# Optimization experiments

Hardware: AMD Instinct MI355X
Metric: run time of the kernel (lower is better)

Reference implementation:

```python
import jax, jax.numpy as jnp
import numpy as np

D_MODEL = 512
H = 8
D_FF = 2048
EPS = 1e-6
NEG_INF = -1.0e9


def setup_inputs() -> dict:
    key = jax.random.key(0)
    ks = jax.random.split(key, 12)
    B, S, D, F = 8, 2048, D_MODEL, D_FF
    s = 0.02
    inp = {
        "x": jax.random.normal(ks[0], (B, S, D), jnp.float32),
        "src_mask": jnp.ones((B, 1, 1, S), jnp.int32),
        "w_q": jax.random.normal(ks[1], (D, D), jnp.float32) * s,
        "b_q": jnp.zeros((D,), jnp.float32),
        "w_k": jax.random.normal(ks[2], (D, D), jnp.float32) * s,
        "b_k": jnp.zeros((D,), jnp.float32),
        "w_v": jax.random.normal(ks[3], (D, D), jnp.float32) * s,
        "b_v": jnp.zeros((D,), jnp.float32),
        "w_o": jax.random.normal(ks[4], (D, D), jnp.float32) * s,
        "b_o": jnp.zeros((D,), jnp.float32),
        "w_1": jax.random.normal(ks[5], (F, D), jnp.float32) * s,
        "b_1": jnp.zeros((F,), jnp.float32),
        "w_2": jax.random.normal(ks[6], (D, F), jnp.float32) * s,
        "b_2": jnp.zeros((D,), jnp.float32),
    }
    return inp


def _layer_norm(x):
    # Matches torch: (x - mu) / sqrt(std**2 + eps), std is UNBIASED (ddof=1);
    # alpha/bias params exist in the module but are never applied in forward.
    mu = jnp.mean(x, axis=-1, keepdims=True)
    var = jnp.var(x, axis=-1, keepdims=True, ddof=1)
    return (x - mu) / jnp.sqrt(var + EPS)


def _mha(x, src_mask, w_q, b_q, w_k, b_k, w_v, b_v, w_o, b_o):
    B, S, D = x.shape
    d_k = D // H
    q = x @ w_q.T + b_q
    k = x @ w_k.T + b_k
    v = x @ w_v.T + b_v
    # (B, S, H, d_k) -> (B, H, S, d_k)
    q = q.reshape(B, S, H, d_k).transpose(0, 2, 1, 3)
    k = k.reshape(B, S, H, d_k).transpose(0, 2, 1, 3)
    v = v.reshape(B, S, H, d_k).transpose(0, 2, 1, 3)
    scores = jnp.einsum("bhqd,bhkd->bhqk", q, k) / jnp.sqrt(jnp.float32(d_k))
    scores = jnp.where(src_mask == 0, NEG_INF, scores)
    attn = jax.nn.softmax(scores, axis=-1)  # (B, H, S, S) materialized, as in source
    out = jnp.einsum("bhqk,bhkd->bhqd", attn, v)
    out = out.transpose(0, 2, 1, 3).reshape(B, S, D)
    return out @ w_o.T + b_o


def _ffn(x, w_1, b_1, w_2, b_2):
    return jax.nn.relu(x @ w_1.T + b_1) @ w_2.T + b_2


def reference(x, src_mask, w_q, b_q, w_k, b_k, w_v, b_v, w_o, b_o, w_1, b_1, w_2, b_2):
    # dropout prob = 0.0 -> identity (eval-equivalent)
    x1 = x + _mha(_layer_norm(x), src_mask, w_q, b_q, w_k, b_k, w_v, b_v, w_o, b_o)
    return x1 + _ffn(_layer_norm(x1), w_1, b_1, w_2, b_2)
```

## Files before the change

### kernel.cpp

```cpp
#include <hip/hip_runtime.h>
#include <hip/hip_bf16.h>

typedef unsigned short u16;
typedef __bf16 bf16x8 __attribute__((ext_vector_type(8)));
typedef __bf16 bf16x4 __attribute__((ext_vector_type(4)));
typedef unsigned short u16x8 __attribute__((ext_vector_type(8)));
typedef float f32x4 __attribute__((ext_vector_type(4)));

#define SEQ 2048
#define DMODEL 512
#define NHEAD 8
#define DFF 2048
#define NBATCH 8
#define MROWS (NBATCH * SEQ)

__device__ __forceinline__ u16 f2b(float f) {
    __hip_bfloat16 h = __float2bfloat16(f);
    u16 u;
    __builtin_memcpy(&u, &h, 2);
    return u;
}

__device__ __forceinline__ float ex2(float x) {
#if __has_builtin(__builtin_amdgcn_exp2f)
    return __builtin_amdgcn_exp2f(x);
#else
    return exp2f(x);
#endif
}

__device__ __forceinline__ void gload_lds16(const void* g, void* lds) {
    auto* gp = reinterpret_cast<const __attribute__((address_space(1))) unsigned int*>(
        reinterpret_cast<uintptr_t>(g));
    auto* lp = reinterpret_cast<__attribute__((address_space(3))) unsigned int*>(
        reinterpret_cast<uintptr_t>(lds));
    __builtin_amdgcn_global_load_lds(gp, lp, 16, 0, 0);
}

__global__ __launch_bounds__(256) void cast_weights(
    const float* __restrict__ w0, const float* __restrict__ w1,
    const float* __restrict__ w2, const float* __restrict__ w3,
    const float* __restrict__ w4, const float* __restrict__ w5,
    u16* __restrict__ d0, u16* __restrict__ d1, u16* __restrict__ d2,
    u16* __restrict__ d3, u16* __restrict__ d4, u16* __restrict__ d5) {
    int blk = blockIdx.x;
    const float* s;
    u16* d;
    int base;
    if (blk < 512) {
        int seg = blk >> 7, lb = blk & 127;
        s = seg == 0 ? w0 : seg == 1 ? w1 : seg == 2 ? w2 : w3;
        d = seg == 0 ? d0 : seg == 1 ? d1 : seg == 2 ? d2 : d3;
        base = lb * 2048;
    } else if (blk < 1024) {
        s = w4; d = d4; base = (blk - 512) * 2048;
    } else {
        s = w5; d = d5; base = (blk - 1024) * 2048;
    }
    int i = base + threadIdx.x * 8;
    float4 a = *reinterpret_cast<const float4*>(s + i);
    float4 b = *reinterpret_cast<const float4*>(s + i + 4);
    ushort4 oa, ob;
    oa.x = f2b(a.x); oa.y = f2b(a.y); oa.z = f2b(a.z); oa.w = f2b(a.w);
    ob.x = f2b(b.x); ob.y = f2b(b.y); ob.z = f2b(b.z); ob.w = f2b(b.w);
    *reinterpret_cast<ushort4*>(d + i) = oa;
    *reinterpret_cast<ushort4*>(d + i + 4) = ob;
}

__global__ __launch_bounds__(256) void ln_rows(const float* __restrict__ x,
                                               u16* __restrict__ out) {
    int row = blockIdx.x * 4 + (threadIdx.x >> 6);
    int l = threadIdx.x & 63;
    const float* xr = x + (size_t)row * DMODEL + l * 8;
    float4 a = *reinterpret_cast<const float4*>(xr);
    float4 b = *reinterpret_cast<const float4*>(xr + 4);
    float s = a.x + a.y + a.z + a.w + b.x + b.y + b.z + b.w;
    float q = a.x * a.x + a.y * a.y + a.z * a.z + a.w * a.w +
              b.x * b.x + b.y * b.y + b.z * b.z + b.w * b.w;
#pragma unroll
    for (int d = 32; d >= 1; d >>= 1) {
        s += __shfl_xor(s, d, 64);
        q += __shfl_xor(q, d, 64);
    }
    float mean = s * (1.f / 512.f);
    float var = (q - 512.f * mean * mean) * (1.f / 511.f);
    float rs = rsqrtf(var + 1e-6f);
    ushort4 o0, o1;
    o0.x = f2b((a.x - mean) * rs); o0.y = f2b((a.y - mean) * rs);
    o0.z = f2b((a.z - mean) * rs); o0.w = f2b((a.w - mean) * rs);
    o1.x = f2b((b.x - mean) * rs); o1.y = f2b((b.y - mean) * rs);
    o1.z = f2b((b.z - mean) * rs); o1.w = f2b((b.w - mean) * rs);
    u16* op = out + (size_t)row * DMODEL + l * 8;
    *reinterpret_cast<ushort4*>(op) = o0;
    *reinterpret_cast<ushort4*>(op + 4) = o1;
}

template <bool RELU, bool RESID, int OUTMODE>
__global__ __launch_bounds__(256, 2) void gemm_nt(
    const u16* __restrict__ A, const u16* __restrict__ W,
    const float* __restrict__ bias, const float* __restrict__ resid,
    void* __restrict__ Cout, int N, int K) {
    __shared__ u16 Als[128 * 64];
    __shared__ u16 Bls[128 * 64];
    const int tid = threadIdx.x;
    const int l = tid & 63, w = tid >> 6;
    const int m0 = blockIdx.y * 128;
    const int n0 = blockIdx.x * 128;
    const int wr = (w >> 1) * 64, wc = (w & 1) * 64;
    const int lhi = l >> 4, l15 = l & 15, l7 = l & 7;

    f32x4 acc[4][4] = {};

    const int srow = l >> 3;
    const int scol = ((l & 7) * 8) ^ (srow << 3);

    for (int kt = 0; kt < K; kt += 64) {
        __syncthreads();
#pragma unroll
        for (int i = 0; i < 4; ++i) {
            int cc = w * 4 + i;
            int grow = cc * 8 + srow;
            gload_lds16(&A[(size_t)(m0 + grow) * K + kt + scol], &Als[cc * 512]);
            gload_lds16(&W[(size_t)(n0 + grow) * K + kt + scol], &Bls[cc * 512]);
        }
        __syncthreads();
#pragma unroll
        for (int kk = 0; kk < 2; ++kk) {
            const int koff = (kk * 32 + lhi * 8) ^ (l7 << 3);
            bf16x8 af[4], bfr[4];
#pragma unroll
            for (int m = 0; m < 4; ++m)
                af[m] = *reinterpret_cast<const bf16x8*>(
                    &Als[(wr + m * 16 + l15) * 64 + koff]);
#pragma unroll
            for (int n = 0; n < 4; ++n)
                bfr[n] = *reinterpret_cast<const bf16x8*>(
                    &Bls[(wc + n * 16 + l15) * 64 + koff]);
#pragma unroll
            for (int m = 0; m < 4; ++m)
#pragma unroll
                for (int n = 0; n < 4; ++n)
                    acc[m][n] = __builtin_amdgcn_mfma_f32_16x16x32_bf16(
                        af[m], bfr[n], acc[m][n], 0, 0, 0);
        }
    }

    int colg[4];
    float bv[4];
#pragma unroll
    for (int cn = 0; cn < 4; ++cn) {
        colg[cn] = n0 + wc + cn * 16 + l15;
        bv[cn] = bias[colg[cn]];
    }
#pragma unroll
    for (int am = 0; am < 4; ++am) {
        int rowg = m0 + wr + am * 16 + 4 * lhi;
#pragma unroll
        for (int cn = 0; cn < 4; ++cn) {
            float v[4];
#pragma unroll
            for (int r = 0; r < 4; ++r) {
                float t = acc[am][cn][r] + bv[cn];
                if constexpr (RELU) t = fmaxf(t, 0.f);
                if constexpr (RESID)
                    t += resid[(size_t)(rowg + r) * N + colg[cn]];
                v[r] = t;
            }
            if constexpr (OUTMODE == 0) {
                u16* o = (u16*)Cout;
#pragma unroll
                for (int r = 0; r < 4; ++r)
                    o[(size_t)(rowg + r) * N + colg[cn]] = f2b(v[r]);
            } else if constexpr (OUTMODE == 1) {
                float* o = (float*)Cout;
#pragma unroll
                for (int r = 0; r < 4; ++r)
                    o[(size_t)(rowg + r) * N + colg[cn]] = v[r];
            } else {
                u16* o = (u16*)Cout;
                int bb = rowg >> 11, sloc = rowg & 2047;
                ushort4 pk;
                pk.x = f2b(v[0]); pk.y = f2b(v[1]);
                pk.z = f2b(v[2]); pk.w = f2b(v[3]);
                *reinterpret_cast<ushort4*>(
                    &o[((size_t)(bb * 512 + colg[cn])) * 2048 + sloc]) = pk;
            }
        }
    }
}

__global__ __launch_bounds__(256, 3) void attn_fwd(
    const u16* __restrict__ q, const u16* __restrict__ k,
    const u16* __restrict__ vT, const int* __restrict__ mask,
    u16* __restrict__ out) {
    __shared__ u16 Kls[2][64 * 64];
    __shared__ u16 Vls[2][64 * 64];
    const int tid = threadIdx.x;
    const int l = tid & 63, w = tid >> 6;
    const int lhi = l >> 4, l15 = l & 15;
    const int lb = (blockIdx.x & 7) * 128 + (blockIdx.x >> 3);
    const int qt = lb & 15, bh = lb >> 4;
    const int b = bh >> 3, h = bh & 7;
    const int q0 = qt * 128 + w * 32;

    const u16* Kb = k + (size_t)b * SEQ * DMODEL + h * 64;
    const u16* Vb = vT + ((size_t)b * 512 + h * 64) * SEQ;
    const int* Mb = mask + b * SEQ;

    const int srow = l >> 3;
    const int scol = ((l & 7) ^ srow) << 3;

    bf16x8 qf[2][2];
#pragma unroll
    for (int g = 0; g < 2; ++g) {
        size_t qa = ((size_t)b * SEQ + q0 + g * 16 + l15) * DMODEL + h * 64 + lhi * 8;
        qf[g][0] = *reinterpret_cast<const bf16x8*>(&q[qa]);
        qf[g][1] = *reinterpret_cast<const bf16x8*>(&q[qa + 32]);
    }

    int allone;
    {
        int acc = 1;
#pragma unroll
        for (int i = 0; i < 8; ++i) {
            int4 mm = *reinterpret_cast<const int4*>(&Mb[l * 32 + i * 4]);
            acc &= mm.x & mm.y & mm.z & mm.w;
        }
        allone = __all(acc == 1);
    }

    float mrun[2] = {-1e30f, -1e30f};
    float lrun[2] = {0.f, 0.f};
    f32x4 oacc[2][4] = {};
    const float C1 = 0.18033688f;

    auto stage = [&](int buf, int kv) {
#pragma unroll
        for (int i = 0; i < 2; ++i) {
            int cc = w * 2 + i;
            int row = cc * 8 + srow;
            gload_lds16(&Kb[(size_t)(kv + row) * DMODEL + scol], &Kls[buf][cc * 512]);
            gload_lds16(&Vb[(size_t)row * SEQ + kv + scol], &Vls[buf][cc * 512]);
        }
    };

    stage(0, 0);
    asm volatile("s_waitcnt vmcnt(0)" ::: "memory");
    __builtin_amdgcn_s_barrier();

    for (int t = 0; t < 32; ++t) {
        const int buf = t & 1;
        const int kv = t * 64;
        if (t < 31) stage(buf ^ 1, kv + 64);
        __builtin_amdgcn_sched_barrier(0);

        const int sw = (l15 & 7) << 3;

        f32x4 sc[2][4];
        __builtin_amdgcn_s_setprio(1);
#pragma unroll
        for (int ks = 0; ks < 4; ++ks) {
            int krow = ks * 16 + l15;
            bf16x8 ka0 = *reinterpret_cast<const bf16x8*>(
                &Kls[buf][krow * 64 + ((lhi * 8) ^ sw)]);
            bf16x8 ka1 = *reinterpret_cast<const bf16x8*>(
                &Kls[buf][krow * 64 + ((32 + lhi * 8) ^ sw)]);
#pragma unroll
            for (int g = 0; g < 2; ++g) {
                f32x4 z = {};
                z = __builtin_amdgcn_mfma_f32_16x16x32_bf16(ka0, qf[g][0], z, 0, 0, 0);
                z = __builtin_amdgcn_mfma_f32_16x16x32_bf16(ka1, qf[g][1], z, 0, 0, 0);
                sc[g][ks] = z;
            }
        }
        __builtin_amdgcn_s_setprio(0);

        if (!allone) {
            int4 mm[4];
#pragma unroll
            for (int ks = 0; ks < 4; ++ks)
                mm[ks] = *reinterpret_cast<const int4*>(&Mb[kv + ks * 16 + 4 * lhi]);
#pragma unroll
            for (int ks = 0; ks < 4; ++ks) {
                if (mm[ks].x == 0) { sc[0][ks][0] = -3e38f; sc[1][ks][0] = -3e38f; }
                if (mm[ks].y == 0) { sc[0][ks][1] = -3e38f; sc[1][ks][1] = -3e38f; }
                if (mm[ks].z == 0) { sc[0][ks][2] = -3e38f; sc[1][ks][2] = -3e38f; }
                if (mm[ks].w == 0) { sc[0][ks][3] = -3e38f; sc[1][ks][3] = -3e38f; }
            }
        }

        u16x8 pk[2][2];
#pragma unroll
        for (int g = 0; g < 2; ++g) {
            float mx = -3e38f;
#pragma unroll
            for (int ks = 0; ks < 4; ++ks)
                mx = fmaxf(mx, fmaxf(fmaxf(sc[g][ks][0], sc[g][ks][1]),
                                     fmaxf(sc[g][ks][2], sc[g][ks][3])));
            mx = fmaxf(mx, __shfl_xor(mx, 16, 64));
            mx = fmaxf(mx, __shfl_xor(mx, 32, 64));
            mx *= C1;
            float mn = fmaxf(mrun[g], mx);
            float fr = ex2(mrun[g] - mn);
            mrun[g] = mn;
            float ps = 0.f;
#pragma unroll
            for (int ks = 0; ks < 4; ++ks) {
                float p0 = ex2(fmaf(sc[g][ks][0], C1, -mn));
                float p1 = ex2(fmaf(sc[g][ks][1], C1, -mn));
                float p2 = ex2(fmaf(sc[g][ks][2], C1, -mn));
                float p3 = ex2(fmaf(sc[g][ks][3], C1, -mn));
                ps += (p0 + p1) + (p2 + p3);
                pk[g][ks >> 1][(ks & 1) * 4 + 0] = f2b(p0);
                pk[g][ks >> 1][(ks & 1) * 4 + 1] = f2b(p1);
                pk[g][ks >> 1][(ks & 1) * 4 + 2] = f2b(p2);
                pk[g][ks >> 1][(ks & 1) * 4 + 3] = f2b(p3);
            }
            ps += __shfl_xor(ps, 16, 64);
            ps += __shfl_xor(ps, 32, 64);
            lrun[g] = lrun[g] * fr + ps;
            float frr[4];
#pragma unroll
            for (int r = 0; r < 4; ++r) frr[r] = __shfl(fr, 4 * lhi + r, 16);
#pragma unroll
            for (int dc = 0; dc < 4; ++dc)
#pragma unroll
                for (int r = 0; r < 4; ++r) oacc[g][dc][r] *= frr[r];
        }

        __builtin_amdgcn_s_setprio(1);
#pragma unroll
        for (int kp = 0; kp < 2; ++kp) {
#pragma unroll
            for (int dc = 0; dc < 4; ++dc) {
                int base = (dc * 16 + l15) * 64;
                bf16x4 v0 = *reinterpret_cast<const bf16x4*>(
                    &Vls[buf][base + ((kp * 32 + lhi * 4) ^ sw)]);
                bf16x4 v1 = *reinterpret_cast<const bf16x4*>(
                    &Vls[buf][base + ((kp * 32 + 16 + lhi * 4) ^ sw)]);
                bf16x8 vb8;
                vb8[0] = v0[0]; vb8[1] = v0[1]; vb8[2] = v0[2]; vb8[3] = v0[3];
                vb8[4] = v1[0]; vb8[5] = v1[1]; vb8[6] = v1[2]; vb8[7] = v1[3];
#pragma unroll
                for (int g = 0; g < 2; ++g)
                    oacc[g][dc] = __builtin_amdgcn_mfma_f32_16x16x32_bf16(
                        __builtin_bit_cast(bf16x8, pk[g][kp]), vb8, oacc[g][dc],
                        0, 0, 0);
            }
        }
        __builtin_amdgcn_s_setprio(0);

        asm volatile("s_waitcnt vmcnt(0)" ::: "memory");
        __builtin_amdgcn_s_barrier();
    }

#pragma unroll
    for (int g = 0; g < 2; ++g) {
        float inv = 1.f / lrun[g];
        float invr[4];
#pragma unroll
        for (int r = 0; r < 4; ++r) invr[r] = __shfl(inv, 4 * lhi + r, 16);
#pragma unroll
        for (int r = 0; r < 4; ++r) {
            size_t rowa =
                ((size_t)b * SEQ + q0 + g * 16 + 4 * lhi + r) * DMODEL + h * 64;
#pragma unroll
            for (int dc = 0; dc < 4; ++dc)
                out[rowa + dc * 16 + l15] = f2b(oacc[g][dc][r] * invr[r]);
        }
    }
}

extern "C" void kernel_launch(void* const* d_in, const int* in_sizes, int n_in,
                              void* d_out, int out_size, void* d_ws,
                              size_t ws_size, hipStream_t stream) {
    const float* x = (const float*)d_in[0];
    const int* mask = (const int*)d_in[1];
    const float* w_q = (const float*)d_in[2];
    const float* b_q = (const float*)d_in[3];
    const float* w_k = (const float*)d_in[4];
    const float* b_k = (const float*)d_in[5];
    const float* w_v = (const float*)d_in[6];
    const float* b_v = (const float*)d_in[7];
    const float* w_o = (const float*)d_in[8];
    const float* b_o = (const float*)d_in[9];
    const float* w_1 = (const float*)d_in[10];
    const float* b_1 = (const float*)d_in[11];
    const float* w_2 = (const float*)d_in[12];
    const float* b_2 = (const float*)d_in[13];

    char* ws = (char*)d_ws;
    const size_t MB = 1024ull * 1024ull;
    u16* lnx = (u16*)(ws + 0);
    u16* qb = (u16*)(ws + 16 * MB);
    u16* kb = (u16*)(ws + 32 * MB);
    u16* vT = (u16*)(ws + 48 * MB);
    u16* lnx1 = (u16*)(ws + 16 * MB);
    u16* hbuf = (u16*)(ws + 32 * MB);
    u16* wqb = (u16*)(ws + 96 * MB);
    u16* wkb = wqb + 262144;
    u16* wvb = wqb + 2 * 262144;
    u16* wob = wqb + 3 * 262144;
    u16* w1b = wqb + 4 * 262144;
    u16* w2b = w1b + 1048576;
    u16* attn_o = lnx;
    float* x1 = (float*)d_out;

    cast_weights<<<1536, 256, 0, stream>>>(w_q, w_k, w_v, w_o, w_1, w_2, wqb,
                                           wkb, wvb, wob, w1b, w2b);
    ln_rows<<<4096, 256, 0, stream>>>(x, lnx);

    dim3 g4(4, 128), g16(16, 128);
    gemm_nt<false, false, 0><<<g4, 256, 0, stream>>>(lnx, wqb, b_q, nullptr,
                                                     qb, 512, 512);
    gemm_nt<false, false, 0><<<g4, 256, 0, stream>>>(lnx, wkb, b_k, nullptr,
                                                     kb, 512, 512);
    gemm_nt<false, false, 2><<<g4, 256, 0, stream>>>(lnx, wvb, b_v, nullptr,
                                                     vT, 512, 512);
    attn_fwd<<<1024, 256, 0, stream>>>(qb, kb, vT, mask, attn_o);
    gemm_nt<false, true, 1><<<g4, 256, 0, stream>>>(attn_o, wob, b_o, x, x1,
                                                    512, 512);
    ln_rows<<<4096, 256, 0, stream>>>(x1, lnx1);
    gemm_nt<true, false, 0><<<g16, 256, 0, stream>>>(lnx1, w1b, b_1, nullptr,
                                                     hbuf, 2048, 512);
    gemm_nt<false, true, 1><<<g4, 256, 0, stream>>>(hbuf, w2b, b_2, x1,
                                                    (float*)d_out, 512, 2048);
}
```

Measured before the change: 317.0 us.

## Load K directly to registers, lazily rescale softmax, pack bf16 pairs in attention

The attention kernel no longer stages K through LDS. Each lane loads its K fragments straight into registers, prefetched one tile ahead, and only V keeps the double-buffered LDS path. The online softmax now rescales the running max, sum and output accumulators only when some row's new max exceeds the running max by more than 8 (in log2 units), which skips the exp and multiply work on most tiles. Probabilities are converted to bf16 two at a time, the launch bound is raised to 4 blocks per CU, and the end-of-loop wait no longer drains the outstanding K loads. In exchange there is more register pressure from the K prefetch and uncoalesced-style per-lane global K reads, which may limit the gain from the higher occupancy target.

```diff
diff --git a/kernel.cpp b/kernel.cpp
--- a/kernel.cpp
+++ b/kernel.cpp
@@ -4,7 +4,7 @@
 typedef unsigned short u16;
 typedef __bf16 bf16x8 __attribute__((ext_vector_type(8)));
 typedef __bf16 bf16x4 __attribute__((ext_vector_type(4)));
-typedef unsigned short u16x8 __attribute__((ext_vector_type(8)));
+typedef unsigned int u32x4 __attribute__((ext_vector_type(4)));
 typedef float f32x4 __attribute__((ext_vector_type(4)));
 
 #define SEQ 2048
@@ -18,6 +18,14 @@
     __hip_bfloat16 h = __float2bfloat16(f);
     u16 u;
     __builtin_memcpy(&u, &h, 2);
+    return u;
+}
+
+__device__ __forceinline__ unsigned int pack2(float a, float b) {
+    float2 f{a, b};
+    __hip_bfloat162 h = __float22bfloat162_rn(f);
+    unsigned int u;
+    __builtin_memcpy(&u, &h, 4);
     return u;
 }
 
@@ -189,11 +197,10 @@
     }
 }
 
-__global__ __launch_bounds__(256, 3) void attn_fwd(
+__global__ __launch_bounds__(256, 4) void attn_fwd(
     const u16* __restrict__ q, const u16* __restrict__ k,
     const u16* __restrict__ vT, const int* __restrict__ mask,
     u16* __restrict__ out) {
-    __shared__ u16 Kls[2][64 * 64];
     __shared__ u16 Vls[2][64 * 64];
     const int tid = threadIdx.x;
     const int l = tid & 63, w = tid >> 6;
@@ -234,42 +241,47 @@
     f32x4 oacc[2][4] = {};
     const float C1 = 0.18033688f;
 
-    auto stage = [&](int buf, int kv) {
+    auto stageV = [&](int buf, int kv) {
 #pragma unroll
         for (int i = 0; i < 2; ++i) {
             int cc = w * 2 + i;
             int row = cc * 8 + srow;
-            gload_lds16(&Kb[(size_t)(kv + row) * DMODEL + scol], &Kls[buf][cc * 512]);
             gload_lds16(&Vb[(size_t)row * SEQ + kv + scol], &Vls[buf][cc * 512]);
         }
     };
 
-    stage(0, 0);
+    bf16x8 kf[8];
+    auto loadK = [&](int kv) {
+#pragma unroll
+        for (int ks = 0; ks < 4; ++ks) {
+            const u16* kr = Kb + (size_t)(kv + ks * 16 + l15) * DMODEL + lhi * 8;
+            kf[2 * ks] = *reinterpret_cast<const bf16x8*>(kr);
+            kf[2 * ks + 1] = *reinterpret_cast<const bf16x8*>(kr + 32);
+        }
+    };
+
+    stageV(0, 0);
+    loadK(0);
     asm volatile("s_waitcnt vmcnt(0)" ::: "memory");
     __builtin_amdgcn_s_barrier();
 
     for (int t = 0; t < 32; ++t) {
         const int buf = t & 1;
         const int kv = t * 64;
-        if (t < 31) stage(buf ^ 1, kv + 64);
+        if (t < 31) stageV(buf ^ 1, kv + 64);
         __builtin_amdgcn_sched_barrier(0);
-
-        const int sw = (l15 & 7) << 3;
 
         f32x4 sc[2][4];
         __builtin_amdgcn_s_setprio(1);
 #pragma unroll
         for (int ks = 0; ks < 4; ++ks) {
-            int krow = ks * 16 + l15;
-            bf16x8 ka0 = *reinterpret_cast<const bf16x8*>(
-                &Kls[buf][krow * 64 + ((lhi * 8) ^ sw)]);
-            bf16x8 ka1 = *reinterpret_cast<const bf16x8*>(
-                &Kls[buf][krow * 64 + ((32 + lhi * 8) ^ sw)]);
 #pragma unroll
             for (int g = 0; g < 2; ++g) {
                 f32x4 z = {};
-                z = __builtin_amdgcn_mfma_f32_16x16x32_bf16(ka0, qf[g][0], z, 0, 0, 0);
-                z = __builtin_amdgcn_mfma_f32_16x16x32_bf16(ka1, qf[g][1], z, 0, 0, 0);
+                z = __builtin_amdgcn_mfma_f32_16x16x32_bf16(kf[2 * ks], qf[g][0],
+                                                            z, 0, 0, 0);
+                z = __builtin_amdgcn_mfma_f32_16x16x32_bf16(kf[2 * ks + 1],
+                                                            qf[g][1], z, 0, 0, 0);
                 sc[g][ks] = z;
             }
         }
@@ -289,20 +301,45 @@
             }
         }
 
-        u16x8 pk[2][2];
+        if (t < 31) loadK(kv + 64);
+
+        float pm[2];
 #pragma unroll
         for (int g = 0; g < 2; ++g) {
-            float mx = -3e38f;
-#pragma unroll
-            for (int ks = 0; ks < 4; ++ks)
-                mx = fmaxf(mx, fmaxf(fmaxf(sc[g][ks][0], sc[g][ks][1]),
-                                     fmaxf(sc[g][ks][2], sc[g][ks][3])));
+            float mx = fmaxf(fmaxf(fmaxf(sc[g][0][0], sc[g][0][1]),
+                                   fmaxf(sc[g][0][2], sc[g][0][3])),
+                             fmaxf(fmaxf(sc[g][1][0], sc[g][1][1]),
+                                   fmaxf(sc[g][1][2], sc[g][1][3])));
+            float mx2 = fmaxf(fmaxf(fmaxf(sc[g][2][0], sc[g][2][1]),
+                                    fmaxf(sc[g][2][2], sc[g][2][3])),
+                              fmaxf(fmaxf(sc[g][3][0], sc[g][3][1]),
+                                    fmaxf(sc[g][3][2], sc[g][3][3])));
+            mx = fmaxf(mx, mx2);
             mx = fmaxf(mx, __shfl_xor(mx, 16, 64));
             mx = fmaxf(mx, __shfl_xor(mx, 32, 64));
-            mx *= C1;
-            float mn = fmaxf(mrun[g], mx);
-            float fr = ex2(mrun[g] - mn);
-            mrun[g] = mn;
+            pm[g] = mx * C1;
+        }
+        if (__any((pm[0] > mrun[0] + 8.f) || (pm[1] > mrun[1] + 8.f))) {
+#pragma unroll
+            for (int g = 0; g < 2; ++g) {
+                float mn = fmaxf(mrun[g], pm[g]);
+                float fr = ex2(mrun[g] - mn);
+                mrun[g] = mn;
+                lrun[g] *= fr;
+                float frr[4];
+#pragma unroll
+                for (int r = 0; r < 4; ++r) frr[r] = __shfl(fr, 4 * lhi + r, 16);
+#pragma unroll
+                for (int dc = 0; dc < 4; ++dc)
+#pragma unroll
+                    for (int r = 0; r < 4; ++r) oacc[g][dc][r] *= frr[r];
+            }
+        }
+
+        u32x4 pku[2][2];
+#pragma unroll
+        for (int g = 0; g < 2; ++g) {
+            float mn = mrun[g];
             float ps = 0.f;
 #pragma unroll
             for (int ks = 0; ks < 4; ++ks) {
@@ -311,23 +348,15 @@
                 float p2 = ex2(fmaf(sc[g][ks][2], C1, -mn));
                 float p3 = ex2(fmaf(sc[g][ks][3], C1, -mn));
                 ps += (p0 + p1) + (p2 + p3);
-                pk[g][ks >> 1][(ks & 1) * 4 + 0] = f2b(p0);
-                pk[g][ks >> 1][(ks & 1) * 4 + 1] = f2b(p1);
-                pk[g][ks >> 1][(ks & 1) * 4 + 2] = f2b(p2);
-                pk[g][ks >> 1][(ks & 1) * 4 + 3] = f2b(p3);
+                pku[g][ks >> 1][(ks & 1) * 2 + 0] = pack2(p0, p1);
+                pku[g][ks >> 1][(ks & 1) * 2 + 1] = pack2(p2, p3);
             }
             ps += __shfl_xor(ps, 16, 64);
             ps += __shfl_xor(ps, 32, 64);
-            lrun[g] = lrun[g] * fr + ps;
-            float frr[4];
-#pragma unroll
-            for (int r = 0; r < 4; ++r) frr[r] = __shfl(fr, 4 * lhi + r, 16);
-#pragma unroll
-            for (int dc = 0; dc < 4; ++dc)
-#pragma unroll
-                for (int r = 0; r < 4; ++r) oacc[g][dc][r] *= frr[r];
-        }
-
+            lrun[g] += ps;
+        }
+
+        const int sw = (l15 & 7) << 3;
         __builtin_amdgcn_s_setprio(1);
 #pragma unroll
         for (int kp = 0; kp < 2; ++kp) {
@@ -344,13 +373,13 @@
 #pragma unroll
                 for (int g = 0; g < 2; ++g)
                     oacc[g][dc] = __builtin_amdgcn_mfma_f32_16x16x32_bf16(
-                        __builtin_bit_cast(bf16x8, pk[g][kp]), vb8, oacc[g][dc],
+                        __builtin_bit_cast(bf16x8, pku[g][kp]), vb8, oacc[g][dc],
                         0, 0, 0);
             }
         }
         __builtin_amdgcn_s_setprio(0);
 
-        asm volatile("s_waitcnt vmcnt(0)" ::: "memory");
+        asm volatile("s_waitcnt vmcnt(8)" ::: "memory");
         __builtin_amdgcn_s_barrier();
     }
 
```

Result: slower. 462.6 us (+46.0%).
